# Kernel optimization log

Measured on AMD Instinct MI355X. Metric: run time of the kernel, lower is better.

The kernel has to match this reference:

```python
import jax, jax.numpy as jnp
import numpy as np

HID = 128   # Config.hidden_dim
K = 16      # kNN neighbors in TempEdgeConv
BIG = 1e9


def _glu(x, wl, bl, wg, bg):
    return (x @ wl + bl) * jax.nn.sigmoid(x @ wg + bg)


def _temp_edge_conv(h, t, w, b, k):
    # h: [G,n,d] node features, t: [G,n,1] temporal key feature
    # dynamic kNN graph on temporal distance within each graph
    d = jnp.abs(t - jnp.swapaxes(t, 1, 2))                  # [G,n,n]
    n = h.shape[1]
    d = d + jnp.eye(n, dtype=h.dtype) * BIG                  # exclude self
    _, idx = jax.lax.top_k(-d, k)                            # [G,n,k]
    hj = jax.vmap(lambda hg, ig: hg[ig])(h, idx)             # [G,n,k,d] gather
    hi = jnp.broadcast_to(h[:, :, None, :], hj.shape)
    e = jnp.concatenate([hi, hj - hi], axis=-1)              # [G,n,k,2d]
    e = e @ w + b                                            # edge MLP
    return jnp.max(e, axis=2)                                # max aggregation


def setup_inputs():
    key = jax.random.key(0)
    ks = jax.random.split(key, 18)
    G, n, IN, H = 64, 1024, 17, HID
    N = G * n
    feat = IN - 1                  # 16
    temb = H // 4                  # 32

    def lin(k1, i, o):
        ka, kb = jax.random.split(k1)
        return (jax.random.normal(ka, (i, o), jnp.float32) / np.sqrt(i),
                jax.random.normal(kb, (o,), jnp.float32) * 0.01)

    x = jax.random.normal(ks[0], (N, IN), jnp.float32)
    batch = jnp.repeat(jnp.arange(G, dtype=jnp.int32), n)
    te_w, te_b = lin(ks[1], 1, temb)
    ig_lw, ig_lb = lin(ks[2], feat + temb, H)
    ig_gw, ig_gb = lin(ks[3], feat + temb, H)
    c1_w, c1_b = lin(ks[4], 2 * H, H)
    c2_w, c2_b = lin(ks[5], 2 * H, H)
    fg_lw, fg_lb = lin(ks[6], 4 * H, H)
    fg_gw, fg_gb = lin(ks[7], 4 * H, H)
    out_w, out_b = lin(ks[8], H, 2)
    return {"x": x, "te_w": te_w, "te_b": te_b,
            "ig_lw": ig_lw, "ig_lb": ig_lb, "ig_gw": ig_gw, "ig_gb": ig_gb,
            "c1_w": c1_w, "c1_b": c1_b, "c2_w": c2_w, "c2_b": c2_b,
            "fg_lw": fg_lw, "fg_lb": fg_lb, "fg_gw": fg_gw, "fg_gb": fg_gb,
            "out_w": out_w, "out_b": out_b,
            "batch": batch, "num_graphs": 64}


def reference(x, te_w, te_b, ig_lw, ig_lb, ig_gw, ig_gb,
              c1_w, c1_b, c2_w, c2_b, fg_lw, fg_lb, fg_gw, fg_gb,
              out_w, out_b, batch, num_graphs):
    G = int(num_graphs)
    N = x.shape[0]
    n = N // G   # equal-sized graphs (batch = repeat(arange(G), n))
    key_feat = x[:, :1]                       # key_feature_idx == 0
    feats = x[:, 1:]
    t_emb = key_feat @ te_w + te_b            # time encoder [N, H//4]
    h = _glu(jnp.concatenate([feats, t_emb], axis=-1),
             ig_lw, ig_lb, ig_gw, ig_gb)      # [N, H] (dropout = identity, eval)
    h = h.reshape(G, n, HID)
    t = key_feat.reshape(G, n, 1)
    x1 = jax.nn.relu(_temp_edge_conv(h, t, c1_w, c1_b, K))   # [G,n,H]
    x2 = jax.nn.relu(_temp_edge_conv(x1, t, c2_w, c2_b, K))  # [G,n,H]
    comb = jnp.concatenate([x1, x2], axis=-1)                # [G,n,2H]
    pooled = jnp.concatenate([comb.max(axis=1), comb.mean(axis=1)], axis=-1)  # [G,4H]
    logits = _glu(pooled, fg_lw, fg_lb, fg_gw, fg_gb) @ out_w + out_b
    return jax.nn.log_softmax(logits, axis=-1)
```

## Files before the change

kernel.cpp:

```cpp
#include <hip/hip_runtime.h>
#include <math.h>

#define NN 65536
#define NG 64
#define NPG 1024
#define HID 128
#define KNN 16
#define BINF 1e30f
#define BWS 272

typedef unsigned long long ull;
typedef _Float16 f16;
typedef _Float16 f16x8 __attribute__((ext_vector_type(8)));
typedef float f32x4 __attribute__((ext_vector_type(4)));

__global__ __launch_bounds__(1024) void k_topk(
    const float* __restrict__ x, int* __restrict__ sidxg,
    short* __restrict__ nbroff,
    const float* __restrict__ ig_lw, const float* __restrict__ ig_gw,
    const float* __restrict__ c1_w, const float* __restrict__ c2_w,
    f16* __restrict__ gfrag, f16* __restrict__ f1, f16* __restrict__ f2) {
    __shared__ ull key[1024];
    __shared__ float st[1024];
    __shared__ int sidx[1024];
    int g = blockIdx.x;
    if (g >= NG) {
        int gid = (g - NG) * 1024 + threadIdx.x;
        if (gid < 16384) {
            int i = gid & 7, lane = (gid >> 3) & 63, nt = (gid >> 9) & 7;
            int kt = (gid >> 12) & 1, mat = gid >> 13;
            int k = kt * 32 + ((lane >> 4) << 3) + i;
            int c = nt * 16 + (lane & 15);
            float v = 0.0f;
            if (k < 48) v = (mat ? ig_gw : ig_lw)[k * 128 + c];
            gfrag[gid] = (f16)v;
        } else {
            int g2 = gid - 16384;
            int buf = g2 >> 15;
            int rem = g2 & 32767;
            int mat = rem >> 14;
            int r2 = rem & 16383;
            int i = r2 & 7, lane = (r2 >> 3) & 63, nt = (r2 >> 9) & 7, kt = (r2 >> 12) & 3;
            int k = kt * 32 + ((lane >> 4) << 3) + i;
            int c = nt * 16 + (lane & 15);
            const float* cw = buf ? c2_w : c1_w;
            float top = cw[k * 128 + c];
            float bot = cw[(128 + k) * 128 + c];
            float v = mat ? bot : (top - bot);
            (buf ? f2 : f1)[rem] = (f16)v;
        }
        return;
    }
    int i = threadIdx.x;
    float t = x[(size_t)(g * NPG + i) * 17];
    unsigned ub = __float_as_uint(t);
    ub = (ub & 0x80000000u) ? ~ub : (ub | 0x80000000u);
    ull kk = ((ull)ub << 32) | (unsigned)i;

    for (int k = 2; k <= 1024; k <<= 1) {
        for (int j = k >> 1; j > 0; j >>= 1) {
            ull pv;
            if (j >= 64) {
                key[i] = kk;
                __syncthreads();
                pv = key[i ^ j];
                __syncthreads();
            } else {
                pv = __shfl_xor(kk, j, 64);
            }
            bool up = ((i & k) == 0);
            bool low = ((i & j) == 0);
            ull mn = kk < pv ? kk : pv;
            ull mx = kk < pv ? pv : kk;
            kk = (up == low) ? mn : mx;
        }
    }
    int oi = (int)(kk & 0xffffffffu);
    st[i] = x[(size_t)(g * NPG + oi) * 17];
    sidx[i] = oi;
    sidxg[g * NPG + i] = g * NPG + oi;
    __syncthreads();

    float tt = st[i];
    int L = i - 1, R = i + 1;
    short* out = nbroff + (size_t)(g * NPG + i) * KNN;
#pragma unroll
    for (int q = 0; q < KNN; q++) {
        float dl = (L >= 0)   ? (tt - st[L]) : BINF;
        float dr = (R < NPG) ? (st[R] - tt) : BINF;
        bool left;
        if (dl < dr) left = true;
        else if (dr < dl) left = false;
        else left = (sidx[L] < sidx[R]);
        int jr;
        if (left) { jr = L; L--; }
        else      { jr = R; R++; }
        out[q] = (short)((jr - i) * BWS);
    }
}

__global__ __launch_bounds__(256) void k_fuse1(
    const float* __restrict__ x, const float* __restrict__ te_w,
    const float* __restrict__ te_b, const f16x8* __restrict__ gfrag,
    const float* __restrict__ bl, const float* __restrict__ bg,
    const int* __restrict__ sidxg, const f16x8* __restrict__ wfrag,
    const float* __restrict__ cb, f16* __restrict__ A, f16* __restrict__ B) {
    __shared__ f16x8 XL[4 * 2 * 64];
    __shared__ f16 ht[64 * 128];
    int tid = threadIdx.x;
    int r0 = blockIdx.x * 64;
#pragma unroll
    for (int p = 0; p < 2; p++) {
        int idx = tid + p * 256;
        int row = idx >> 3, kq = idx & 7;
        int node = sidxg[r0 + row];
        f16x8 h;
        if (kq < 2) {
            const float* xr = x + (size_t)node * 17 + 1 + kq * 8;
#pragma unroll
            for (int i = 0; i < 8; i++) h[i] = (f16)xr[i];
        } else if (kq < 6) {
            float t = x[(size_t)node * 17];
            int j0 = (kq - 2) * 8;
#pragma unroll
            for (int i = 0; i < 8; i++) h[i] = (f16)fmaf(t, te_w[j0 + i], te_b[j0 + i]);
        } else {
#pragma unroll
            for (int i = 0; i < 8; i++) h[i] = (f16)0.0f;
        }
        int mf = row >> 4, kt = kq >> 2, lane = ((kq & 3) << 4) | (row & 15);
        XL[(mf * 2 + kt) * 64 + lane] = h;
    }
    __syncthreads();
    int w = tid >> 6, lane = tid & 63;
    f32x4 acc[2][2][4];
#pragma unroll
    for (int o = 0; o < 2; o++)
#pragma unroll
        for (int j = 0; j < 2; j++)
#pragma unroll
            for (int mf = 0; mf < 4; mf++) acc[o][j][mf] = (f32x4){0.f, 0.f, 0.f, 0.f};
#pragma unroll 1
    for (int kt = 0; kt < 2; kt++) {
        f16x8 wf0[2], wf1[2], xa[4];
#pragma unroll
        for (int j = 0; j < 2; j++) {
            wf0[j] = gfrag[((0 * 2 + kt) * 8 + (w * 2 + j)) * 64 + lane];
            wf1[j] = gfrag[((1 * 2 + kt) * 8 + (w * 2 + j)) * 64 + lane];
        }
#pragma unroll
        for (int mf = 0; mf < 4; mf++) xa[mf] = XL[(mf * 2 + kt) * 64 + lane];
#pragma unroll
        for (int mf = 0; mf < 4; mf++)
#pragma unroll
            for (int j = 0; j < 2; j++) {
                acc[0][j][mf] = __builtin_amdgcn_mfma_f32_16x16x32_f16(xa[mf], wf0[j], acc[0][j][mf], 0, 0, 0);
                acc[1][j][mf] = __builtin_amdgcn_mfma_f32_16x16x32_f16(xa[mf], wf1[j], acc[1][j][mf], 0, 0, 0);
            }
    }
#pragma unroll
    for (int j = 0; j < 2; j++) {
        int col = w * 32 + j * 16 + (lane & 15);
        float bbl = bl[col], bbg = bg[col];
#pragma unroll
        for (int mf = 0; mf < 4; mf++) {
            int rloc = mf * 16 + ((lane >> 4) << 2);
#pragma unroll
            for (int q = 0; q < 4; q++) {
                float lin = acc[0][j][mf][q] + bbl;
                float gat = acc[1][j][mf][q] + bbg;
                int row = rloc + q;
                ht[(row * 128 + col) ^ ((row & 7) << 3)] = (f16)(lin / (1.0f + expf(-gat)));
            }
        }
    }
    __syncthreads();
#pragma unroll
    for (int o = 0; o < 2; o++)
#pragma unroll
        for (int j = 0; j < 2; j++)
#pragma unroll
            for (int mf = 0; mf < 4; mf++) acc[o][j][mf] = (f32x4){0.f, 0.f, 0.f, 0.f};
    int row16 = lane & 15, kslot = lane >> 4;
    int swz = (row16 & 7) << 3;
#pragma unroll 1
    for (int kt = 0; kt < 4; kt++) {
        f16x8 wf0[2], wf1[2], xa[4];
#pragma unroll
        for (int j = 0; j < 2; j++) {
            wf0[j] = wfrag[((0 * 4 + kt) * 8 + (w * 2 + j)) * 64 + lane];
            wf1[j] = wfrag[((1 * 4 + kt) * 8 + (w * 2 + j)) * 64 + lane];
        }
#pragma unroll
        for (int mf = 0; mf < 4; mf++)
            xa[mf] = *(const f16x8*)&ht[((mf * 16 + row16) * 128 + kt * 32 + kslot * 8) ^ swz];
#pragma unroll
        for (int mf = 0; mf < 4; mf++)
#pragma unroll
            for (int j = 0; j < 2; j++) {
                acc[0][j][mf] = __builtin_amdgcn_mfma_f32_16x16x32_f16(xa[mf], wf0[j], acc[0][j][mf], 0, 0, 0);
                acc[1][j][mf] = __builtin_amdgcn_mfma_f32_16x16x32_f16(xa[mf], wf1[j], acc[1][j][mf], 0, 0, 0);
            }
    }
#pragma unroll
    for (int j = 0; j < 2; j++) {
        int col = w * 32 + j * 16 + (lane & 15);
        float bias = cb[col];
#pragma unroll
        for (int mf = 0; mf < 4; mf++) {
            int rbase = r0 + mf * 16 + ((lane >> 4) << 2);
#pragma unroll
            for (int q = 0; q < 4; q++) {
                A[(size_t)(rbase + q) * 128 + col] = (f16)(acc[0][j][mf][q] + bias);
                B[(size_t)(rbase + q) * 128 + col] = (f16)acc[1][j][mf][q];
            }
        }
    }
}

__global__ __launch_bounds__(256) void k_megac2(
    const f16* __restrict__ A1, const f16* __restrict__ B1,
    const short* __restrict__ nbroff, const f16x8* __restrict__ wfrag,
    const float* __restrict__ cb,
    float* __restrict__ partM1, float* __restrict__ partS1,
    float* __restrict__ partM2, float* __restrict__ partS2) {
    __shared__ char SM[80896];
    char* bw  = SM;
    char* b2  = SM;
    f16*  x1t = (f16*)(SM + 34816);
    char* a2  = SM + 59392;
    float* redM = (float*)(SM + 76800);
    float* redS = (float*)(SM + 78848);

    int tid = threadIdx.x;
    int bx = blockIdx.x;
    int r0 = bx * 64;
    int r0loc = (bx & 15) * 64;
    int gbase = r0 - r0loc;

#pragma unroll
    for (int p = 0; p < 8; p++) {
        int idx = tid + p * 256;
        int row = idx >> 4, kq = idx & 15;
        int gl = r0loc - 32 + row;
        f16x8 v;
#pragma unroll
        for (int i = 0; i < 8; i++) v[i] = (f16)0.0f;
        if (gl >= 0 && gl < NPG)
            v = *(const f16x8*)(B1 + (size_t)(gbase + gl) * 128 + kq * 8);
        *(f16x8*)(bw + row * BWS + kq * 16) = v;
    }
    __syncthreads();

    int w = tid >> 6, lane = tid & 63;
    int rquad = lane >> 4;
    int c0 = (lane & 15) * 8;

    f16x8 pmv;
    float ps[8];
#pragma unroll
    for (int i = 0; i < 8; i++) { pmv[i] = (f16)(-INFINITY); ps[i] = 0.f; }
#pragma unroll 2
    for (int rr = 0; rr < 6; rr++) {
        int row = w * 24 + rr * 4 + rquad;
        int gl = r0loc - 16 + row;
        f16x8 ou;
#pragma unroll
        for (int i = 0; i < 8; i++) ou[i] = (f16)0.0f;
        if (gl >= 0 && gl < NPG) {
            int grow = gbase + gl;
            const int4* op = (const int4*)(nbroff + (size_t)grow * KNN);
            int4 oa = op[0], ob = op[1];
            short ow[16];
            *(int4*)ow = oa; *(int4*)(ow + 8) = ob;
            f16x8 av = *(const f16x8*)(A1 + (size_t)grow * 128 + c0);
            f16x8 m;
#pragma unroll
            for (int i = 0; i < 8; i++) m[i] = (f16)(-INFINITY);
            const char* base = bw + (row + 16) * BWS + c0 * 2;
#pragma unroll
            for (int q = 0; q < 16; q++) {
                f16x8 bv = *(const f16x8*)(base + (int)ow[q]);
                m = __builtin_elementwise_max(m, bv);
            }
            f16x8 z = {(f16)0, (f16)0, (f16)0, (f16)0, (f16)0, (f16)0, (f16)0, (f16)0};
            ou = __builtin_elementwise_max(av + m, z);
            if ((row >= 16) && (row < 80)) {
                pmv = __builtin_elementwise_max(pmv, ou);
#pragma unroll
                for (int i = 0; i < 8; i++) ps[i] += (float)ou[i];
            }
        }
        int idx = (row * 128 + c0) ^ ((row & 7) << 3);
        *(f16x8*)&x1t[idx] = ou;
    }
    float pm[8];
#pragma unroll
    for (int i = 0; i < 8; i++) pm[i] = (float)pmv[i];
#pragma unroll
    for (int i = 0; i < 8; i++) {
        pm[i] = fmaxf(pm[i], __shfl_xor(pm[i], 16));
        pm[i] = fmaxf(pm[i], __shfl_xor(pm[i], 32));
        ps[i] += __shfl_xor(ps[i], 16);
        ps[i] += __shfl_xor(ps[i], 32);
    }
    if (rquad == 0) {
#pragma unroll
        for (int i = 0; i < 8; i++) {
            redM[w * 128 + c0 + i] = pm[i];
            redS[w * 128 + c0 + i] = ps[i];
        }
    }
    __syncthreads();
    if (tid < 128) {
        float M = -BINF, S = 0.f;
#pragma unroll
        for (int w2 = 0; w2 < 4; w2++) {
            M = fmaxf(M, redM[w2 * 128 + tid]);
            S += redS[w2 * 128 + tid];
        }
        partM1[(size_t)bx * 128 + tid] = M;
        partS1[(size_t)bx * 128 + tid] = S;
    }

    f32x4 acc[2][2][6];
#pragma unroll
    for (int o = 0; o < 2; o++)
#pragma unroll
        for (int j = 0; j < 2; j++)
#pragma unroll
            for (int mf = 0; mf < 6; mf++) acc[o][j][mf] = (f32x4){0.f, 0.f, 0.f, 0.f};
    int row16 = lane & 15, kslot = lane >> 4;
    int swz = (row16 & 7) << 3;
#pragma unroll 1
    for (int kt = 0; kt < 4; kt++) {
        f16x8 wf0[2], wf1[2], xa[6];
#pragma unroll
        for (int j = 0; j < 2; j++) {
            wf0[j] = wfrag[((0 * 4 + kt) * 8 + (w * 2 + j)) * 64 + lane];
            wf1[j] = wfrag[((1 * 4 + kt) * 8 + (w * 2 + j)) * 64 + lane];
        }
#pragma unroll
        for (int mf = 0; mf < 6; mf++)
            xa[mf] = *(const f16x8*)&x1t[((mf * 16 + row16) * 128 + kt * 32 + kslot * 8) ^ swz];
#pragma unroll
        for (int mf = 0; mf < 6; mf++)
#pragma unroll
            for (int j = 0; j < 2; j++) {
                acc[0][j][mf] = __builtin_amdgcn_mfma_f32_16x16x32_f16(xa[mf], wf0[j], acc[0][j][mf], 0, 0, 0);
                acc[1][j][mf] = __builtin_amdgcn_mfma_f32_16x16x32_f16(xa[mf], wf1[j], acc[1][j][mf], 0, 0, 0);
            }
    }
#pragma unroll
    for (int j = 0; j < 2; j++) {
        int col = w * 32 + j * 16 + (lane & 15);
        float bias = cb[col];
#pragma unroll
        for (int mf = 0; mf < 6; mf++) {
            int rloc = mf * 16 + ((lane >> 4) << 2);
#pragma unroll
            for (int q = 0; q < 4; q++) {
                int hrow = rloc + q;
                *(f16*)(b2 + hrow * BWS + col * 2) = (f16)acc[1][j][mf][q];
                if (hrow >= 16 && hrow < 80)
                    *(f16*)(a2 + (hrow - 16) * BWS + col * 2) = (f16)(acc[0][j][mf][q] + bias);
            }
        }
    }
    __syncthreads();

#pragma unroll
    for (int i = 0; i < 8; i++) { pmv[i] = (f16)(-INFINITY); ps[i] = 0.f; }
#pragma unroll 2
    for (int rr = 0; rr < 4; rr++) {
        int rl = w * 16 + rr * 4 + rquad;
        int grow = r0 + rl;
        const int4* op = (const int4*)(nbroff + (size_t)grow * KNN);
        int4 oa = op[0], ob = op[1];
        short ow[16];
        *(int4*)ow = oa; *(int4*)(ow + 8) = ob;
        f16x8 av = *(const f16x8*)(a2 + rl * BWS + c0 * 2);
        f16x8 m;
#pragma unroll
        for (int i = 0; i < 8; i++) m[i] = (f16)(-INFINITY);
        const char* base = b2 + (rl + 16) * BWS + c0 * 2;
#pragma unroll
        for (int q = 0; q < 16; q++) {
            f16x8 bv = *(const f16x8*)(base + (int)ow[q]);
            m = __builtin_elementwise_max(m, bv);
        }
        f16x8 z = {(f16)0, (f16)0, (f16)0, (f16)0, (f16)0, (f16)0, (f16)0, (f16)0};
        f16x8 v = __builtin_elementwise_max(av + m, z);
        pmv = __builtin_elementwise_max(pmv, v);
#pragma unroll
        for (int i = 0; i < 8; i++) ps[i] += (float)v[i];
    }
#pragma unroll
    for (int i = 0; i < 8; i++) pm[i] = (float)pmv[i];
#pragma unroll
    for (int i = 0; i < 8; i++) {
        pm[i] = fmaxf(pm[i], __shfl_xor(pm[i], 16));
        pm[i] = fmaxf(pm[i], __shfl_xor(pm[i], 32));
        ps[i] += __shfl_xor(ps[i], 16);
        ps[i] += __shfl_xor(ps[i], 32);
    }
    __syncthreads();
    if (rquad == 0) {
#pragma unroll
        for (int i = 0; i < 8; i++) {
            redM[w * 128 + c0 + i] = pm[i];
            redS[w * 128 + c0 + i] = ps[i];
        }
    }
    __syncthreads();
    if (tid < 128) {
        float M = -BINF, S = 0.f;
#pragma unroll
        for (int w2 = 0; w2 < 4; w2++) {
            M = fmaxf(M, redM[w2 * 128 + tid]);
            S += redS[w2 * 128 + tid];
        }
        partM2[(size_t)bx * 128 + tid] = M;
        partS2[(size_t)bx * 128 + tid] = S;
    }
}

__global__ __launch_bounds__(256) void k_final(const float* __restrict__ partM1,
                                               const float* __restrict__ partS1,
                                               const float* __restrict__ partM2,
                                               const float* __restrict__ partS2,
                                               const float* __restrict__ fg_lw,
                                               const float* __restrict__ fg_lb,
                                               const float* __restrict__ fg_gw,
                                               const float* __restrict__ fg_gb,
                                               const float* __restrict__ out_w,
                                               const float* __restrict__ out_b,
                                               float* __restrict__ out) {
    __shared__ float pooled[512];
    __shared__ float linv[128], gatev[128];
    __shared__ float gluv[128];
    __shared__ float lg[2];
    int g = blockIdx.x, tid = threadIdx.x;

    const float* pM = (tid < 128) ? partM1 : partM2;
    const float* pS = (tid < 128) ? partS1 : partS2;
    int cc = tid & 127;
    float mx = -BINF, sm = 0.0f;
    for (int ch = 0; ch < 16; ch++) {
        mx = fmaxf(mx, pM[(size_t)(g * 16 + ch) * 128 + cc]);
        sm += pS[(size_t)(g * 16 + ch) * 128 + cc];
    }
    pooled[tid] = mx;
    pooled[256 + tid] = sm * (1.0f / 1024.0f);
    __syncthreads();

    float acc = 0.0f;
    if (tid < 128) {
        for (int k = 0; k < 512; k++) acc = fmaf(pooled[k], fg_lw[k * 128 + tid], acc);
        linv[tid] = acc + fg_lb[tid];
    } else {
        int c = tid - 128;
        for (int k = 0; k < 512; k++) acc = fmaf(pooled[k], fg_gw[k * 128 + c], acc);
        gatev[c] = acc + fg_gb[c];
    }
    __syncthreads();
    if (tid < 128) gluv[tid] = linv[tid] / (1.0f + expf(-gatev[tid]));
    __syncthreads();
    if (tid < 2) {
        float s = out_b[tid];
        for (int c = 0; c < 128; c++) s = fmaf(gluv[c], out_w[c * 2 + tid], s);
        lg[tid] = s;
    }
    __syncthreads();
    if (tid < 2) {
        float m = fmaxf(lg[0], lg[1]);
        float lse = m + logf(expf(lg[0] - m) + expf(lg[1] - m));
        out[g * 2 + tid] = lg[tid] - lse;
    }
}

extern "C" void kernel_launch(void* const* d_in, const int* in_sizes, int n_in,
                              void* d_out, int out_size, void* d_ws, size_t ws_size,
                              hipStream_t stream) {
    const float* x     = (const float*)d_in[0];
    const float* te_w  = (const float*)d_in[1];
    const float* te_b  = (const float*)d_in[2];
    const float* ig_lw = (const float*)d_in[3];
    const float* ig_lb = (const float*)d_in[4];
    const float* ig_gw = (const float*)d_in[5];
    const float* ig_gb = (const float*)d_in[6];
    const float* c1_w  = (const float*)d_in[7];
    const float* c1_b  = (const float*)d_in[8];
    const float* c2_w  = (const float*)d_in[9];
    const float* c2_b  = (const float*)d_in[10];
    const float* fg_lw = (const float*)d_in[11];
    const float* fg_lb = (const float*)d_in[12];
    const float* fg_gw = (const float*)d_in[13];
    const float* fg_gb = (const float*)d_in[14];
    const float* out_w = (const float*)d_in[15];
    const float* out_b = (const float*)d_in[16];
    float* out = (float*)d_out;

    char* p = (char*)d_ws;
    const size_t T16 = (size_t)NN * HID * sizeof(f16);
    f16* A1 = (f16*)p; p += T16;
    f16* B1 = (f16*)p; p += T16;
    int* sidxg = (int*)p;            p += (size_t)NN * 4;
    short* nbroff = (short*)p;       p += (size_t)NN * KNN * 2;
    float* partM1 = (float*)p;       p += (size_t)1024 * 128 * 4;
    float* partS1 = (float*)p;       p += (size_t)1024 * 128 * 4;
    float* partM2 = (float*)p;       p += (size_t)1024 * 128 * 4;
    float* partS2 = (float*)p;       p += (size_t)1024 * 128 * 4;
    f16* gfrag = (f16*)p;            p += 16384 * 2;
    f16* f1 = (f16*)p;               p += 32768 * 2;
    f16* f2 = (f16*)p;               p += 32768 * 2;

    k_topk<<<NG + 80, 1024, 0, stream>>>(x, sidxg, nbroff, ig_lw, ig_gw,
                                         c1_w, c2_w, gfrag, f1, f2);
    k_fuse1<<<NN / 64, 256, 0, stream>>>(x, te_w, te_b, (const f16x8*)gfrag,
                                         ig_lb, ig_gb, sidxg, (const f16x8*)f1,
                                         c1_b, A1, B1);
    k_megac2<<<NN / 64, 256, 0, stream>>>(A1, B1, nbroff, (const f16x8*)f2,
                                          c2_b, partM1, partS1, partM2, partS2);
    k_final<<<NG, 256, 0, stream>>>(partM1, partS1, partM2, partS2,
                                    fg_lw, fg_lb, fg_gw, fg_gb, out_w, out_b, out);
}
```

Baseline: 107.4 us.

## Double k_megac2 block size to 512 threads and reuse LDS for reductions

Grows k_megac2 from 4 to 8 waves per block, each handling half the rows in the gather/max phases and half the output columns in the MFMA phase. The reduction scratch buffers now alias dead regions of the shared buffer, shrinking LDS per block, and an extra barrier guards that reuse. The aim is more waves in flight per CU to hide LDS and global latency in the gather loops. The cost is an extra sync, less per-wave work to amortise fixed overhead, and loops no longer unrolled.

Measured after the change: 103.3 us. 1.04x faster.

```diff
diff --git a/kernel.cpp b/kernel.cpp
--- a/kernel.cpp
+++ b/kernel.cpp
@@ -218,19 +218,21 @@
     }
 }
 
-__global__ __launch_bounds__(256) void k_megac2(
+__global__ __launch_bounds__(512) void k_megac2(
     const f16* __restrict__ A1, const f16* __restrict__ B1,
     const short* __restrict__ nbroff, const f16x8* __restrict__ wfrag,
     const float* __restrict__ cb,
     float* __restrict__ partM1, float* __restrict__ partS1,
     float* __restrict__ partM2, float* __restrict__ partS2) {
-    __shared__ char SM[80896];
+    __shared__ char SM[76800];
     char* bw  = SM;
     char* b2  = SM;
     f16*  x1t = (f16*)(SM + 34816);
     char* a2  = SM + 59392;
-    float* redM = (float*)(SM + 76800);
-    float* redS = (float*)(SM + 78848);
+    float* redM1 = (float*)(SM + 59392);
+    float* redS1 = (float*)(SM + 63488);
+    float* redM2 = (float*)(SM + 34816);
+    float* redS2 = (float*)(SM + 38912);
 
     int tid = threadIdx.x;
     int bx = blockIdx.x;
@@ -239,8 +241,8 @@
     int gbase = r0 - r0loc;
 
 #pragma unroll
-    for (int p = 0; p < 8; p++) {
-        int idx = tid + p * 256;
+    for (int p = 0; p < 4; p++) {
+        int idx = tid + p * 512;
         int row = idx >> 4, kq = idx & 15;
         int gl = r0loc - 32 + row;
         f16x8 v;
@@ -260,9 +262,9 @@
     float ps[8];
 #pragma unroll
     for (int i = 0; i < 8; i++) { pmv[i] = (f16)(-INFINITY); ps[i] = 0.f; }
-#pragma unroll 2
-    for (int rr = 0; rr < 6; rr++) {
-        int row = w * 24 + rr * 4 + rquad;
+#pragma unroll 1
+    for (int rr = 0; rr < 3; rr++) {
+        int row = w * 12 + rr * 4 + rquad;
         int gl = r0loc - 16 + row;
         f16x8 ou;
 #pragma unroll
@@ -307,53 +309,46 @@
     if (rquad == 0) {
 #pragma unroll
         for (int i = 0; i < 8; i++) {
-            redM[w * 128 + c0 + i] = pm[i];
-            redS[w * 128 + c0 + i] = ps[i];
+            redM1[w * 128 + c0 + i] = pm[i];
+            redS1[w * 128 + c0 + i] = ps[i];
         }
     }
     __syncthreads();
     if (tid < 128) {
         float M = -BINF, S = 0.f;
 #pragma unroll
-        for (int w2 = 0; w2 < 4; w2++) {
-            M = fmaxf(M, redM[w2 * 128 + tid]);
-            S += redS[w2 * 128 + tid];
+        for (int w2 = 0; w2 < 8; w2++) {
+            M = fmaxf(M, redM1[w2 * 128 + tid]);
+            S += redS1[w2 * 128 + tid];
         }
         partM1[(size_t)bx * 128 + tid] = M;
         partS1[(size_t)bx * 128 + tid] = S;
     }
-
-    f32x4 acc[2][2][6];
+    __syncthreads();
+
+    f32x4 acc[2][6];
 #pragma unroll
     for (int o = 0; o < 2; o++)
 #pragma unroll
-        for (int j = 0; j < 2; j++)
-#pragma unroll
-            for (int mf = 0; mf < 6; mf++) acc[o][j][mf] = (f32x4){0.f, 0.f, 0.f, 0.f};
+        for (int mf = 0; mf < 6; mf++) acc[o][mf] = (f32x4){0.f, 0.f, 0.f, 0.f};
     int row16 = lane & 15, kslot = lane >> 4;
     int swz = (row16 & 7) << 3;
 #pragma unroll 1
     for (int kt = 0; kt < 4; kt++) {
-        f16x8 wf0[2], wf1[2], xa[6];
-#pragma unroll
-        for (int j = 0; j < 2; j++) {
-            wf0[j] = wfrag[((0 * 4 + kt) * 8 + (w * 2 + j)) * 64 + lane];
-            wf1[j] = wfrag[((1 * 4 + kt) * 8 + (w * 2 + j)) * 64 + lane];
-        }
+        f16x8 wf0, wf1, xa[6];
+        wf0 = wfrag[((0 * 4 + kt) * 8 + w) * 64 + lane];
+        wf1 = wfrag[((1 * 4 + kt) * 8 + w) * 64 + lane];
 #pragma unroll
         for (int mf = 0; mf < 6; mf++)
             xa[mf] = *(const f16x8*)&x1t[((mf * 16 + row16) * 128 + kt * 32 + kslot * 8) ^ swz];
 #pragma unroll
-        for (int mf = 0; mf < 6; mf++)
-#pragma unroll
-            for (int j = 0; j < 2; j++) {
-                acc[0][j][mf] = __builtin_amdgcn_mfma_f32_16x16x32_f16(xa[mf], wf0[j], acc[0][j][mf], 0, 0, 0);
-                acc[1][j][mf] = __builtin_amdgcn_mfma_f32_16x16x32_f16(xa[mf], wf1[j], acc[1][j][mf], 0, 0, 0);
-            }
-    }
-#pragma unroll
-    for (int j = 0; j < 2; j++) {
-        int col = w * 32 + j * 16 + (lane & 15);
+        for (int mf = 0; mf < 6; mf++) {
+            acc[0][mf] = __builtin_amdgcn_mfma_f32_16x16x32_f16(xa[mf], wf0, acc[0][mf], 0, 0, 0);
+            acc[1][mf] = __builtin_amdgcn_mfma_f32_16x16x32_f16(xa[mf], wf1, acc[1][mf], 0, 0, 0);
+        }
+    }
+    {
+        int col = w * 16 + (lane & 15);
         float bias = cb[col];
 #pragma unroll
         for (int mf = 0; mf < 6; mf++) {
@@ -361,9 +356,9 @@
 #pragma unroll
             for (int q = 0; q < 4; q++) {
                 int hrow = rloc + q;
-                *(f16*)(b2 + hrow * BWS + col * 2) = (f16)acc[1][j][mf][q];
+                *(f16*)(b2 + hrow * BWS + col * 2) = (f16)acc[1][mf][q];
                 if (hrow >= 16 && hrow < 80)
-                    *(f16*)(a2 + (hrow - 16) * BWS + col * 2) = (f16)(acc[0][j][mf][q] + bias);
+                    *(f16*)(a2 + (hrow - 16) * BWS + col * 2) = (f16)(acc[0][mf][q] + bias);
             }
         }
     }
@@ -371,9 +366,9 @@
 
 #pragma unroll
     for (int i = 0; i < 8; i++) { pmv[i] = (f16)(-INFINITY); ps[i] = 0.f; }
-#pragma unroll 2
-    for (int rr = 0; rr < 4; rr++) {
-        int rl = w * 16 + rr * 4 + rquad;
+#pragma unroll 1
+    for (int rr = 0; rr < 2; rr++) {
+        int rl = w * 8 + rr * 4 + rquad;
         int grow = r0 + rl;
         const int4* op = (const int4*)(nbroff + (size_t)grow * KNN);
         int4 oa = op[0], ob = op[1];
@@ -408,17 +403,17 @@
     if (rquad == 0) {
 #pragma unroll
         for (int i = 0; i < 8; i++) {
-            redM[w * 128 + c0 + i] = pm[i];
-            redS[w * 128 + c0 + i] = ps[i];
+            redM2[w * 128 + c0 + i] = pm[i];
+            redS2[w * 128 + c0 + i] = ps[i];
         }
     }
     __syncthreads();
     if (tid < 128) {
         float M = -BINF, S = 0.f;
 #pragma unroll
-        for (int w2 = 0; w2 < 4; w2++) {
-            M = fmaxf(M, redM[w2 * 128 + tid]);
-            S += redS[w2 * 128 + tid];
+        for (int w2 = 0; w2 < 8; w2++) {
+            M = fmaxf(M, redM2[w2 * 128 + tid]);
+            S += redS2[w2 * 128 + tid];
         }
         partM2[(size_t)bx * 128 + tid] = M;
         partS2[(size_t)bx * 128 + tid] = S;
@@ -520,7 +515,7 @@
     k_fuse1<<<NN / 64, 256, 0, stream>>>(x, te_w, te_b, (const f16x8*)gfrag,
                                          ig_lb, ig_gb, sidxg, (const f16x8*)f1,
                                          c1_b, A1, B1);
-    k_megac2<<<NN / 64, 256, 0, stream>>>(A1, B1, nbroff, (const f16x8*)f2,
+    k_megac2<<<NN / 64, 512, 0, stream>>>(A1, B1, nbroff, (const f16x8*)f2,
                                           c2_b, partM1, partS1, partM2, partS2);
     k_final<<<NG, 256, 0, stream>>>(partM1, partS1, partM2, partS2,
                                     fg_lw, fg_lb, fg_gw, fg_gb, out_w, out_b, out);
```
